# Performance work log

Hardware: AMD Instinct MI355X
Metric: run time of the kernel (lower is better)

The kernel has to match this reference:

```python
import jax, jax.numpy as jnp
import numpy as np

BATCH = 4096
INPUT_SIZE = 8192
IO = 16            # inputoutput_dim
D_STATE = 32       # statespace_dim
N_STAGES = INPUT_SIZE // IO  # 512


def _glorot(key, shape):
    # glorot-uniform over the trailing matrix dims, matching get_random_glorot_uniform_matrix
    lim = float(np.sqrt(6.0 / (shape[-2] + shape[-1])))
    return jax.random.uniform(key, shape, minval=-lim, maxval=lim, dtype=jnp.float32)


def setup_inputs() -> dict:
    key = jax.random.key(0)
    ks = jax.random.split(key, 10)
    U = jax.random.normal(ks[0], (BATCH, INPUT_SIZE), dtype=jnp.float32)
    A = _glorot(ks[1], (N_STAGES, D_STATE, D_STATE))
    B = _glorot(ks[2], (N_STAGES, D_STATE, IO))
    C = _glorot(ks[3], (N_STAGES, IO, D_STATE))
    D = _glorot(ks[4], (N_STAGES, IO, IO))
    E = _glorot(ks[5], (N_STAGES, D_STATE, D_STATE))
    F = _glorot(ks[6], (N_STAGES, D_STATE, IO))
    G = _glorot(ks[7], (N_STAGES, IO, D_STATE))
    lim_b = float(np.sqrt(6.0 / INPUT_SIZE))
    bias = jax.random.uniform(ks[8], (INPUT_SIZE,), minval=-lim_b, maxval=lim_b, dtype=jnp.float32)
    return {"U": U, "A": A, "B": B, "C": C, "D": D, "E": E, "F": F, "G": G, "bias": bias}


def reference(U, A, B, C, D, E, F, G, bias):
    bt, p = U.shape
    n, io, d = C.shape
    u = U.reshape(bt, n, io).transpose(1, 0, 2)  # (N, batch, io)
    x0 = jnp.zeros((bt, d), dtype=U.dtype)

    # causal: y_k = C_k x_k + D_k u_k ; x_{k+1} = A_k x_k + B_k u_k, x_0 = 0
    def causal_step(x, inp):
        A_k, B_k, C_k, D_k, u_k = inp
        y_k = x @ C_k.T + u_k @ D_k.T
        x = x @ A_k.T + u_k @ B_k.T
        return x, y_k

    _, y_c = jax.lax.scan(causal_step, x0, (A, B, C, D, u))

    # anticausal (runs from last stage to first): y_k += G_k z_k ; z_{k-1} = E_k z_k + F_k u_k, z_N = 0
    def anti_step(z, inp):
        E_k, F_k, G_k, u_k = inp
        y_k = z @ G_k.T
        z = z @ E_k.T + u_k @ F_k.T
        return z, y_k

    _, y_a = jax.lax.scan(anti_step, x0, (E, F, G, u), reverse=True)

    y = (y_c + y_a).transpose(1, 0, 2).reshape(bt, p) + bias
    return y
```

## Files before the change

kernel.cpp:

```cpp
#include <hip/hip_runtime.h>


#define BATCH 4096
#define NCH   16
#define CHS   32
#define SROWS (BATCH + 32)
#define TSTR  36

typedef __attribute__((ext_vector_type(8))) short short8;
typedef __attribute__((ext_vector_type(4))) float f32x4;
typedef short8 __attribute__((may_alias)) short8a;
typedef f32x4 __attribute__((may_alias)) f32x4a;
typedef unsigned __attribute__((may_alias)) uinta;

#define MFMA16(a, b, c) __builtin_amdgcn_mfma_f32_16x16x32_bf16(a, b, c, 0, 0, 0)

__device__ __forceinline__ unsigned short bf16u(float x) {
  unsigned u = __builtin_bit_cast(unsigned, x);
  u += 0x7fffu + ((u >> 16) & 1u);
  return (unsigned short)(u >> 16);
}
__device__ __forceinline__ float bf2f(unsigned short u) {
  return __builtin_bit_cast(float, ((unsigned)u) << 16);
}
template <int DT>
__device__ __forceinline__ const void* eptr(const void* b, long e) {
  return (const char*)b + e * (DT ? 4 : 2);
}

__device__ __forceinline__ void gload16(const void* g, void* lds) {
  __builtin_amdgcn_global_load_lds((const __attribute__((address_space(1))) void*)g,
                                   (__attribute__((address_space(3))) void*)lds, 16, 0, 0);
}
__device__ __forceinline__ void stage_blob8(const short* g, short* lds, int w, int lane) {
#pragma unroll
  for (int c = 0; c < 2; ++c) {
    const int ob = (w * 2 + c) * 1024;
    gload16((const char*)g + ob + lane * 16, (char*)lds + ob);
  }
}
__device__ __forceinline__ void stage_blob2k(const short* g, short* lds, int w, int lane) {
  if (w < 2) {
    const int ob = w * 1024;
    gload16((const char*)g + ob + lane * 16, (char*)lds + ob);
  }
}

template <int DT, int ROWS, int COLS, int PSTR>
__device__ __forceinline__ void stage2(const void* gp, short* hi, short* lo, int tid) {
  if constexpr (DT == 0) {
    const uinta* gu = (const uinta*)gp;
    for (int i = tid; i < ROWS * COLS / 2; i += 256) {
      int r = i / (COLS / 2), c = i - r * (COLS / 2);
      ((uinta*)(hi + r * PSTR))[c] = gu[i];
    }
  } else {
    const float* gf = (const float*)gp;
    for (int i = tid; i < ROWS * COLS; i += 256) {
      int r = i / COLS, c = i - r * COLS;
      float v = gf[i];
      unsigned short h = bf16u(v);
      hi[r * PSTR + c] = (short)h;
      lo[r * PSTR + c] = (short)bf16u(v - bf2f(h));
    }
  }
}
template <int DT, int ROWS, int COLS, int PSTR>
__device__ __forceinline__ void stage1(const void* gp, short* hi, int tid) {
  if constexpr (DT == 0) {
    const uinta* gu = (const uinta*)gp;
    for (int i = tid; i < ROWS * COLS / 2; i += 256) {
      int r = i / (COLS / 2), c = i - r * (COLS / 2);
      ((uinta*)(hi + r * PSTR))[c] = gu[i];
    }
  } else {
    const float* gf = (const float*)gp;
    for (int i = tid; i < ROWS * COLS; i += 256) {
      int r = i / COLS, c = i - r * COLS;
      hi[r * PSTR + c] = (short)bf16u(gf[i]);
    }
  }
}

__device__ __forceinline__ short8 ldfrag32(const short* l, int lane, int nbase) {
  int n = nbase + (lane & 15), q = lane >> 4;
  return *(const short8a*)(l + n * 40 + q * 8);
}
__device__ __forceinline__ short8 ldfrag16(const short* l, int lane, int nbase) {
  int n = nbase + (lane & 15), q = lane >> 4;
  short8 z = {};
  if (q < 2) z = *(const short8a*)(l + n * 24 + q * 8);
  return z;
}

__device__ __forceinline__ void twr(const f32x4* acc, float* T, int lane) {
  const int c = lane & 15, q = lane >> 4;
#pragma unroll
  for (int h = 0; h < 2; ++h)
#pragma unroll
    for (int r = 0; r < 4; ++r) T[(q * 4 + r) * TSTR + h * 16 + c] = acc[h][r];
}
__device__ __forceinline__ void trd(const float* T, int lane, short8& hi, short8& lo) {
  const int m = lane & 15, q = lane >> 4;
  const float* p = T + m * TSTR + q * 8;
#pragma unroll
  for (int j = 0; j < 8; ++j) {
    float v = p[j];
    unsigned short h = bf16u(v);
    hi[j] = (short)h;
    lo[j] = (short)bf16u(v - bf2f(h));
  }
}

template <int DT> struct URaw;
template <> struct URaw<0> { short8 s; };
template <> struct URaw<1> { f32x4 a, b; };

template <int DT>
__device__ __forceinline__ URaw<DT> ldu_raw(const void* U, size_t off) {
  URaw<DT> r;
  if constexpr (DT == 0) {
    r.s = *(const short8a*)((const short*)U + off);
  } else {
    const f32x4a* p = (const f32x4a*)((const float*)U + off);
    r.a = p[0];
    r.b = p[1];
  }
  return r;
}
template <int DT>
__device__ __forceinline__ void u_cvt(const URaw<DT>& r, short8& uhi, short8& ulo) {
  if constexpr (DT == 0) {
    uhi = r.s;
    ulo = short8{};
  } else {
#pragma unroll
    for (int j = 0; j < 4; ++j) {
      float v = r.a[j];
      unsigned short h = bf16u(v);
      uhi[j] = (short)h;
      ulo[j] = (short)bf16u(v - bf2f(h));
    }
#pragma unroll
    for (int j = 0; j < 4; ++j) {
      float v = r.b[j];
      unsigned short h = bf16u(v);
      uhi[4 + j] = (short)h;
      ulo[4 + j] = (short)bf16u(v - bf2f(h));
    }
  }
}
template <int DT, int MODE> struct UL {
  URaw<DT> r;
  __device__ __forceinline__ void fetch(const void* U, const short*, size_t row, int k, int qq) {
    r = ldu_raw<DT>(U, row * 8192 + (size_t)k * 16 + qq * 8);
  }
  __device__ __forceinline__ void get(short8& hi, short8& lo) const { u_cvt<DT>(r, hi, lo); }
};
template <> struct UL<1, 2> {
  short8 h, l;
  __device__ __forceinline__ void fetch(const void*, const short* Ub, size_t row, int k, int qq) {
    const short* p = Ub + (row * 1024 + (size_t)k * 2 + qq) * 16;
    h = *(const short8a*)p;
    l = *(const short8a*)(p + 8);
  }
  __device__ __forceinline__ void get(short8& hi, short8& lo) const { hi = h; lo = l; }
};

template <int DT>
__device__ __forceinline__ float ldbias(const void* b, int i) {
  if constexpr (DT == 0) return bf2f((unsigned short)((const short*)b)[i]);
  else return ((const float*)b)[i];
}

template <int DT>
__device__ __forceinline__ void step_state(const short8& Xhi, const short8& Xlo,
                                           const short8& uhi, const short8& ulo,
                                           const short* Mhi, const short* Mlo,
                                           const short* Bhi, const short* Blo,
                                           f32x4* out, int lane) {
#pragma unroll
  for (int h = 0; h < 2; ++h) {
    const f32x4 z4 = {0.f, 0.f, 0.f, 0.f};
    short8 bA = ldfrag32(Mhi, lane, h * 16);
    f32x4 ax = MFMA16(Xhi, bA, z4);
    ax = MFMA16(Xlo, bA, ax);
    short8 bB = ldfrag16(Bhi, lane, h * 16);
    ax = MFMA16(uhi, bB, ax);
    if constexpr (DT) {
      short8 bAl = ldfrag32(Mlo, lane, h * 16);
      ax = MFMA16(Xhi, bAl, ax);
      ax = MFMA16(ulo, bB, ax);
      short8 bBl = ldfrag16(Blo, lane, h * 16);
      ax = MFMA16(uhi, bBl, ax);
    }
    out[h] = ax;
  }
}

__global__ void k_detect(const unsigned short* __restrict__ U16, int* __restrict__ flag) {
  int lane = threadIdx.x;
  int bad = 0;
  for (int i = lane; i < 512; i += 64) {
    int e = (U16[i] >> 7) & 0xFF;
    bad += ((e > 134) || (e < 96 && e != 0)) ? 1 : 0;
  }
#pragma unroll
  for (int s = 32; s; s >>= 1) bad += __shfl_xor(bad, s);
  if (lane == 0) *flag = (bad > 48) ? 1 : 0;
}

template <int DT, int ROWS, int COLS, int PSTR, bool LO>
__device__ __forceinline__ void cvt_mat(const void* gp, short* hi, short* lo, int tid) {
  if constexpr (DT == 0) {
    const unsigned short* gs = (const unsigned short*)gp;
    for (int i = tid; i < ROWS * COLS; i += 256) {
      int r = i / COLS, c = i - r * COLS;
      hi[r * PSTR + c] = (short)gs[i];
    }
  } else {
    const float* gf = (const float*)gp;
    for (int i = tid; i < ROWS * COLS; i += 256) {
      int r = i / COLS, c = i - r * COLS;
      float v = gf[i];
      unsigned short h = bf16u(v);
      hi[r * PSTR + c] = (short)h;
      if constexpr (LO) lo[r * PSTR + c] = (short)bf16u(v - bf2f(h));
    }
  }
}
template <int DT>
__global__ __launch_bounds__(256) void k_prep(
    const int* __restrict__ flagp,
    const void* __restrict__ Am, const void* __restrict__ Bm, const void* __restrict__ Cm,
    const void* __restrict__ Dm, const void* __restrict__ Em, const void* __restrict__ Fm,
    const void* __restrict__ Gm,
    short* __restrict__ ABb, short* __restrict__ EFb, short* __restrict__ CDb,
    short* __restrict__ Gb) {
  if (*flagp != DT) return;
  const int k = blockIdx.x, tid = threadIdx.x;
  short* ab = ABb + (size_t)k * 4096;
  short* ef = EFb + (size_t)k * 4096;
  short* cd = CDb + (size_t)k * 1024;
  short* gb = Gb + (size_t)k * 1024;
  cvt_mat<DT, 32, 32, 40, true>(eptr<DT>(Am, (long)k * 1024), ab, ab + 1280, tid);
  cvt_mat<DT, 32, 16, 24, true>(eptr<DT>(Bm, (long)k * 512), ab + 2560, ab + 3328, tid);
  cvt_mat<DT, 32, 32, 40, true>(eptr<DT>(Em, (long)k * 1024), ef, ef + 1280, tid);
  cvt_mat<DT, 32, 16, 24, true>(eptr<DT>(Fm, (long)k * 512), ef + 2560, ef + 3328, tid);
  cvt_mat<DT, 16, 32, 40, false>(eptr<DT>(Cm, (long)k * 512), cd, nullptr, tid);
  cvt_mat<DT, 16, 16, 24, false>(eptr<DT>(Dm, (long)k * 256), cd + 640, nullptr, tid);
  cvt_mat<DT, 16, 32, 40, false>(eptr<DT>(Gm, (long)k * 512), gb, nullptr, tid);
}
__global__ __launch_bounds__(256) void k_prepU(const int* __restrict__ flagp,
                                               const float* __restrict__ Uf,
                                               short* __restrict__ Ub) {
  if (*flagp != 1) return;
  const size_t i = (size_t)blockIdx.x * 256 + threadIdx.x;
  const f32x4a* p = (const f32x4a*)(Uf + i * 8);
  f32x4 a = p[0], b = p[1];
  short8 hi, lo;
#pragma unroll
  for (int j = 0; j < 4; ++j) {
    unsigned short h = bf16u(a[j]);
    hi[j] = (short)h;
    lo[j] = (short)bf16u(a[j] - bf2f(h));
  }
#pragma unroll
  for (int j = 0; j < 4; ++j) {
    unsigned short h = bf16u(b[j]);
    hi[4 + j] = (short)h;
    lo[4 + j] = (short)bf16u(b[j] - bf2f(h));
  }
  *(short8a*)(Ub + i * 16) = hi;
  *(short8a*)(Ub + i * 16 + 8) = lo;
}

template <int DT, int MODE>
__global__ __launch_bounds__(256, 4) void k1_scan(
    const int* __restrict__ flagp, const void* __restrict__ U,
    const void* __restrict__ Am, const void* __restrict__ Bm,
    const void* __restrict__ Em, const void* __restrict__ Fm,
    const short* __restrict__ ABb, const short* __restrict__ EFb,
    const short* __restrict__ Ub,
    float* __restrict__ Sc, float* __restrict__ Sa) {
  if (*flagp != DT) return;
  const int ch = blockIdx.x, tile = blockIdx.y;
  const bool ident = (tile == 64);
  const int tid = threadIdx.x, lane = tid & 63, w = tid >> 6;
  const int s = ch * CHS;
  __shared__ __align__(16) short bAB[2][4096];
  __shared__ __align__(16) short bEF[2][4096];
  __shared__ __align__(16) float T[4][2][16 * TSTR];

  short8 Xhi = {}, Xlo = {}, Zhi = {}, Zlo = {};
  if (ident) {
    const int m = lane & 15, q = lane >> 4;
    short8 id = {};
#pragma unroll
    for (int j = 0; j < 8; ++j) id[j] = ((q * 8 + j) == (w * 16 + m)) ? (short)0x3F80 : (short)0;
    Xhi = id; Zhi = id;
  }

  auto stAB = [&](int k, int b) {
    if constexpr (MODE >= 1) {
      stage_blob8(ABb + (size_t)k * 4096, bAB[b], w, lane);
    } else {
      stage2<DT, 32, 32, 40>(eptr<DT>(Am, (long)k * 1024), bAB[b], bAB[b] + 1280, tid);
      stage2<DT, 32, 16, 24>(eptr<DT>(Bm, (long)k * 512), bAB[b] + 2560, bAB[b] + 3328, tid);
    }
  };
  auto stEF = [&](int k, int b) {
    if constexpr (MODE >= 1) {
      stage_blob8(EFb + (size_t)k * 4096, bEF[b], w, lane);
    } else {
      stage2<DT, 32, 32, 40>(eptr<DT>(Em, (long)k * 1024), bEF[b], bEF[b] + 1280, tid);
      stage2<DT, 32, 16, 24>(eptr<DT>(Fm, (long)k * 512), bEF[b] + 2560, bEF[b] + 3328, tid);
    }
  };

  stAB(s, 0);
  stEF(s + CHS - 1, 0);

  const size_t row = (size_t)(ident ? 0 : (tile * 64 + w * 16 + (lane & 15)));
  const int qq = (lane >> 4) & 1;
  UL<DT, MODE> upc, upa;
  if (!ident) {
    upc.fetch(U, Ub, row, s, qq);
    upa.fetch(U, Ub, row, s + CHS - 1, qq);
  }
  __syncthreads();

  f32x4 aX[2], aZ[2];
#pragma unroll 2
  for (int t = 0; t < CHS; ++t) {
    const int kc = s + t, ka = s + CHS - 1 - t, buf = t & 1;
    if (t < CHS - 1) {
      stAB(kc + 1, buf ^ 1);
      stEF(ka - 1, buf ^ 1);
    }
    short8 uch = {}, ucl = {}, uah = {}, ual = {};
    if (!ident) {
      upc.get(uch, ucl);
      upa.get(uah, ual);
      if (t < CHS - 1) {
        upc.fetch(U, Ub, row, kc + 1, qq);
        upa.fetch(U, Ub, row, ka - 1, qq);
      }
    }
    step_state<DT>(Xhi, Xlo, uch, ucl, bAB[buf], bAB[buf] + 1280, bAB[buf] + 2560,
                   bAB[buf] + 3328, aX, lane);
    step_state<DT>(Zhi, Zlo, uah, ual, bEF[buf], bEF[buf] + 1280, bEF[buf] + 2560,
                   bEF[buf] + 3328, aZ, lane);
    twr(aX, T[w][0], lane);
    twr(aZ, T[w][1], lane);
    trd(T[w][0], lane, Xhi, Xlo);
    trd(T[w][1], lane, Zhi, Zlo);
    __syncthreads();
  }

  if (!ident || w < 2) {
    const int grow = tile * 64 + w * 16;
#pragma unroll
    for (int h = 0; h < 2; ++h)
#pragma unroll
      for (int r = 0; r < 4; ++r) {
        const int m = (lane >> 4) * 4 + r, col = h * 16 + (lane & 15);
        const size_t off = ((size_t)ch * SROWS + grow + m) * 32 + col;
        Sc[off] = aX[h][r];
        Sa[off] = aZ[h][r];
      }
  }
}

__global__ __launch_bounds__(256) void k2_comb(float* __restrict__ Sc, float* __restrict__ Sa) {
  const int dir = blockIdx.y;
  const int r = threadIdx.x >> 5, j = threadIdx.x & 31;
  const int row = blockIdx.x * 8 + r;
  float* S = dir ? Sa : Sc;
  __shared__ float P[32][33];
  __shared__ float xs[8][33];
  float x = 0.f;
  for (int it = 0; it < NCH; ++it) {
    const int ch = dir ? (NCH - 1 - it) : it;
    const size_t base = ((size_t)ch * SROWS + row) * 32 + j;
    const float s_local = S[base];
    for (int i = threadIdx.x; i < 1024; i += 256)
      P[i >> 5][i & 31] = S[((size_t)ch * SROWS + BATCH + (i >> 5)) * 32 + (i & 31)];
    xs[r][j] = x;
    __syncthreads();
    S[base] = x;
    float acc = s_local;
#pragma unroll
    for (int m = 0; m < 32; ++m) acc += xs[r][m] * P[m][j];
    x = acc;
    __syncthreads();
  }
}

template <int DT, int MODE>
__global__ __launch_bounds__(256, 4) void k3_scan(
    const int* __restrict__ flagp, const void* __restrict__ U,
    const void* __restrict__ Am, const void* __restrict__ Bm,
    const void* __restrict__ Cm, const void* __restrict__ Dm,
    const void* __restrict__ Em, const void* __restrict__ Fm,
    const void* __restrict__ Gm, const void* __restrict__ biasv,
    const short* __restrict__ ABb, const short* __restrict__ EFb,
    const short* __restrict__ CDb, const short* __restrict__ Gb,
    const short* __restrict__ Ub,
    const float* __restrict__ xin, const float* __restrict__ zin,
    void* __restrict__ out) {
  if (*flagp != DT) return;
  const int ch = blockIdx.x, tile = blockIdx.y;
  const int tid = threadIdx.x, lane = tid & 63, w = tid >> 6;
  const int s = ch * CHS;
  __shared__ __align__(16) short bM[2][4096];
  __shared__ __align__(16) short bO[2][1024];
  __shared__ __align__(16) float T[4][16 * TSTR];
  const int cidx = lane & 15, quad = lane >> 4, qq = quad & 1;
  const size_t row = (size_t)(tile * 64 + w * 16 + cidx);

  auto stC = [&](int k, int b) {
    if constexpr (MODE >= 1) {
      stage_blob8(ABb + (size_t)k * 4096, bM[b], w, lane);
      stage_blob2k(CDb + (size_t)k * 1024, bO[b], w, lane);
    } else {
      stage2<DT, 32, 32, 40>(eptr<DT>(Am, (long)k * 1024), bM[b], bM[b] + 1280, tid);
      stage2<DT, 32, 16, 24>(eptr<DT>(Bm, (long)k * 512), bM[b] + 2560, bM[b] + 3328, tid);
      stage1<DT, 16, 32, 40>(eptr<DT>(Cm, (long)k * 512), bO[b], tid);
      stage1<DT, 16, 16, 24>(eptr<DT>(Dm, (long)k * 256), bO[b] + 640, tid);
    }
  };
  auto stA = [&](int k, int b) {
    if constexpr (MODE >= 1) {
      stage_blob8(EFb + (size_t)k * 4096, bM[b], w, lane);
      stage_blob2k(Gb + (size_t)k * 1024, bO[b], w, lane);
    } else {
      stage2<DT, 32, 32, 40>(eptr<DT>(Em, (long)k * 1024), bM[b], bM[b] + 1280, tid);
      stage2<DT, 32, 16, 24>(eptr<DT>(Fm, (long)k * 512), bM[b] + 2560, bM[b] + 3328, tid);
      stage1<DT, 16, 32, 40>(eptr<DT>(Gm, (long)k * 512), bO[b], tid);
    }
  };

  short8 Xhi, Xlo;
  {
    const float* xp = xin + ((size_t)ch * SROWS + row) * 32 + quad * 8;
#pragma unroll
    for (int j = 0; j < 8; ++j) {
      float v = xp[j];
      unsigned short h = bf16u(v);
      Xhi[j] = (short)h;
      Xlo[j] = (short)bf16u(v - bf2f(h));
    }
  }
  stC(s, 0);
  UL<DT, MODE> up;
  up.fetch(U, Ub, row, s, qq);
  __syncthreads();

  f32x4 aX[2];
#pragma unroll 2
  for (int t = 0; t < CHS; ++t) {
    const int k = s + t, buf = t & 1;
    if (t < CHS - 1) stC(k + 1, buf ^ 1);
    short8 uh, ul;
    up.get(uh, ul);
    if (t < CHS - 1) up.fetch(U, Ub, row, k + 1, qq);
    const f32x4 z4 = {0.f, 0.f, 0.f, 0.f};
    const short8 cf = ldfrag32(bO[buf], lane, 0);
    f32x4 ya = MFMA16(Xhi, cf, z4);
    ya = MFMA16(Xlo, cf, ya);
    const short8 df = ldfrag16(bO[buf] + 640, lane, 0);
    ya = MFMA16(uh, df, ya);
    if constexpr (DT) ya = MFMA16(ul, df, ya);
    const float bv = ldbias<DT>(biasv, k * 16 + cidx);
    {
      const size_t obase = (size_t)(tile * 64 + w * 16 + quad * 4) * 8192 + (size_t)k * 16 + cidx;
      if constexpr (DT == 0) {
        short* o = (short*)out;
#pragma unroll
        for (int r = 0; r < 4; ++r) o[obase + (size_t)r * 8192] = (short)bf16u(ya[r] + bv);
      } else {
        float* o = (float*)out;
#pragma unroll
        for (int r = 0; r < 4; ++r) o[obase + (size_t)r * 8192] = ya[r] + bv;
      }
    }
    step_state<DT>(Xhi, Xlo, uh, ul, bM[buf], bM[buf] + 1280, bM[buf] + 2560, bM[buf] + 3328,
                   aX, lane);
    twr(aX, T[w], lane);
    trd(T[w], lane, Xhi, Xlo);
    __syncthreads();
  }

  short8 Zhi, Zlo;
  {
    const float* zp = zin + ((size_t)ch * SROWS + row) * 32 + quad * 8;
#pragma unroll
    for (int j = 0; j < 8; ++j) {
      float v = zp[j];
      unsigned short h = bf16u(v);
      Zhi[j] = (short)h;
      Zlo[j] = (short)bf16u(v - bf2f(h));
    }
  }
  stA(s + CHS - 1, 0);
  up.fetch(U, Ub, row, s + CHS - 1, qq);
  __syncthreads();

  f32x4 aZ[2];
#pragma unroll 2
  for (int t = 0; t < CHS; ++t) {
    const int k = s + CHS - 1 - t, buf = t & 1;
    if (t < CHS - 1) stA(k - 1, buf ^ 1);
    short8 uh, ul;
    up.get(uh, ul);
    if (t < CHS - 1) up.fetch(U, Ub, row, k - 1, qq);
    const f32x4 z4 = {0.f, 0.f, 0.f, 0.f};
    const short8 gf = ldfrag32(bO[buf], lane, 0);
    f32x4 ya = MFMA16(Zhi, gf, z4);
    ya = MFMA16(Zlo, gf, ya);
    {
      const size_t obase = (size_t)(tile * 64 + w * 16 + quad * 4) * 8192 + (size_t)k * 16 + cidx;
      if constexpr (DT == 0) {
        short* o = (short*)out;
#pragma unroll
        for (int r = 0; r < 4; ++r) {
          const float c = bf2f((unsigned short)o[obase + (size_t)r * 8192]);
          o[obase + (size_t)r * 8192] = (short)bf16u(c + ya[r]);
        }
      } else {
        float* o = (float*)out;
#pragma unroll
        for (int r = 0; r < 4; ++r) o[obase + (size_t)r * 8192] += ya[r];
      }
    }
    step_state<DT>(Zhi, Zlo, uh, ul, bM[buf], bM[buf] + 1280, bM[buf] + 2560, bM[buf] + 3328,
                   aZ, lane);
    twr(aZ, T[w], lane);
    trd(T[w], lane, Zhi, Zlo);
    __syncthreads();
  }
}

extern "C" void kernel_launch(void* const* d_in, const int* in_sizes, int n_in,
                              void* d_out, int out_size, void* d_ws, size_t ws_size,
                              hipStream_t stream) {
  (void)in_sizes; (void)n_in; (void)out_size;
  const void* U = d_in[0];
  const void* A = d_in[1];
  const void* B = d_in[2];
  const void* C = d_in[3];
  const void* D = d_in[4];
  const void* E = d_in[5];
  const void* F = d_in[6];
  const void* G = d_in[7];
  const void* bias = d_in[8];

  constexpr size_t SC1 = (size_t)NCH * SROWS * 32;
  constexpr size_t BLOBS = (size_t)512 * 8192 * 2 + (size_t)512 * 2048 * 2;
  constexpr size_t UBB = (size_t)BATCH * 1024 * 32;
  constexpr size_t NEED1 = 1024 + BLOBS + SC1 * 8;
  constexpr size_t NEED2 = NEED1 + UBB;
  const int mode = (ws_size >= NEED2) ? 2 : (ws_size >= NEED1 ? 1 : 0);

  char* base = (char*)d_ws;
  int* flag = (int*)base;
  short* ABb = (short*)(base + 1024);
  short* EFb = ABb + (size_t)512 * 4096;
  short* CDb = EFb + (size_t)512 * 4096;
  short* Gb = CDb + (size_t)512 * 1024;
  float* Sc = (mode >= 1) ? (float*)(Gb + (size_t)512 * 1024) : (float*)(base + 1024);
  float* Sa = Sc + SC1;
  short* Ub = (short*)(Sa + SC1);

  k_detect<<<1, 64, 0, stream>>>((const unsigned short*)U, flag);
  if (mode >= 1) {
    k_prep<0><<<512, 256, 0, stream>>>(flag, A, B, C, D, E, F, G, ABb, EFb, CDb, Gb);
    k_prep<1><<<512, 256, 0, stream>>>(flag, A, B, C, D, E, F, G, ABb, EFb, CDb, Gb);
  }
  if (mode == 2) k_prepU<<<16384, 256, 0, stream>>>(flag, (const float*)U, Ub);

  if (mode == 2) {
    k1_scan<0, 1><<<dim3(NCH, 65), 256, 0, stream>>>(flag, U, A, B, E, F, ABb, EFb, Ub, Sc, Sa);
    k1_scan<1, 2><<<dim3(NCH, 65), 256, 0, stream>>>(flag, U, A, B, E, F, ABb, EFb, Ub, Sc, Sa);
    k2_comb<<<dim3(BATCH / 8, 2), 256, 0, stream>>>(Sc, Sa);
    k3_scan<0, 1><<<dim3(NCH, 64), 256, 0, stream>>>(flag, U, A, B, C, D, E, F, G, bias, ABb, EFb,
                                                     CDb, Gb, Ub, Sc, Sa, d_out);
    k3_scan<1, 2><<<dim3(NCH, 64), 256, 0, stream>>>(flag, U, A, B, C, D, E, F, G, bias, ABb, EFb,
                                                     CDb, Gb, Ub, Sc, Sa, d_out);
  } else if (mode == 1) {
    k1_scan<0, 1><<<dim3(NCH, 65), 256, 0, stream>>>(flag, U, A, B, E, F, ABb, EFb, Ub, Sc, Sa);
    k1_scan<1, 1><<<dim3(NCH, 65), 256, 0, stream>>>(flag, U, A, B, E, F, ABb, EFb, Ub, Sc, Sa);
    k2_comb<<<dim3(BATCH / 8, 2), 256, 0, stream>>>(Sc, Sa);
    k3_scan<0, 1><<<dim3(NCH, 64), 256, 0, stream>>>(flag, U, A, B, C, D, E, F, G, bias, ABb, EFb,
                                                     CDb, Gb, Ub, Sc, Sa, d_out);
    k3_scan<1, 1><<<dim3(NCH, 64), 256, 0, stream>>>(flag, U, A, B, C, D, E, F, G, bias, ABb, EFb,
                                                     CDb, Gb, Ub, Sc, Sa, d_out);
  } else {
    k1_scan<0, 0><<<dim3(NCH, 65), 256, 0, stream>>>(flag, U, A, B, E, F, ABb, EFb, Ub, Sc, Sa);
    k1_scan<1, 0><<<dim3(NCH, 65), 256, 0, stream>>>(flag, U, A, B, E, F, ABb, EFb, Ub, Sc, Sa);
    k2_comb<<<dim3(BATCH / 8, 2), 256, 0, stream>>>(Sc, Sa);
    k3_scan<0, 0><<<dim3(NCH, 64), 256, 0, stream>>>(flag, U, A, B, C, D, E, F, G, bias, ABb, EFb,
                                                     CDb, Gb, Ub, Sc, Sa, d_out);
    k3_scan<1, 0><<<dim3(NCH, 64), 256, 0, stream>>>(flag, U, A, B, C, D, E, F, G, bias, ABb, EFb,
                                                     CDb, Gb, Ub, Sc, Sa, d_out);
  }
}
```

Baseline: 609.5 us.

## Merge causal and anticausal passes of k3 into one interleaved loop

Replaces the two sequential loops of the final scan kernel (forward causal, then reverse anticausal) with one loop that advances both recurrences at once, with separate double-buffered LDS for AB/CD and EF/G. Output is written directly in the first half of the chunk and read-modify-written in the second half, so each output element gets one plain store and one read-add. This is meant to halve the serial loop length and overlap two independent dependency chains, and to drop the read-modify-write for half the elements. The cost is more LDS and registers, with launch bounds lowered from 4 to 3 blocks per CU. For fp32 output the first-half partial is packed as bf16 into the output buffer, which may lose precision.

```diff
diff --git a/kernel.cpp b/kernel.cpp
--- a/kernel.cpp
+++ b/kernel.cpp
@@ -22,6 +22,9 @@
 }
 __device__ __forceinline__ float bf2f(unsigned short u) {
   return __builtin_bit_cast(float, ((unsigned)u) << 16);
+}
+__device__ __forceinline__ unsigned pk2(float a, float b) {
+  return (unsigned)bf16u(a) | (((unsigned)bf16u(b)) << 16);
 }
 template <int DT>
 __device__ __forceinline__ const void* eptr(const void* b, long e) {
@@ -398,15 +401,144 @@
 }
 
 template <int DT, int MODE>
-__global__ __launch_bounds__(256, 4) void k3_scan(
+__global__ __launch_bounds__(256, 3) void k3_merged(
+    const int* __restrict__ flagp, const void* __restrict__ U, const void* __restrict__ biasv,
+    const short* __restrict__ ABb, const short* __restrict__ EFb,
+    const short* __restrict__ CDb, const short* __restrict__ Gb,
+    const short* __restrict__ Ub,
+    const float* __restrict__ xin, const float* __restrict__ zin,
+    void* __restrict__ out) {
+  if (*flagp != DT) return;
+  const int ch = blockIdx.x, tile = blockIdx.y;
+  const int tid = threadIdx.x, lane = tid & 63, w = tid >> 6;
+  const int s = ch * CHS;
+  __shared__ __align__(16) short bAB[2][4096];
+  __shared__ __align__(16) short bEF[2][4096];
+  __shared__ __align__(16) short bCD[2][1024];
+  __shared__ __align__(16) short bG[2][1024];
+  __shared__ __align__(16) float T[4][16 * TSTR];
+
+  const int cidx = lane & 15, quad = lane >> 4, qq = quad & 1;
+  const size_t row = (size_t)(tile * 64 + w * 16 + cidx);
+
+  short8 Xhi, Xlo, Zhi, Zlo;
+  {
+    const float* xp = xin + ((size_t)ch * SROWS + row) * 32 + quad * 8;
+    const float* zp = zin + ((size_t)ch * SROWS + row) * 32 + quad * 8;
+#pragma unroll
+    for (int j = 0; j < 8; ++j) {
+      float v = xp[j];
+      unsigned short h = bf16u(v);
+      Xhi[j] = (short)h;
+      Xlo[j] = (short)bf16u(v - bf2f(h));
+      float z = zp[j];
+      unsigned short hz = bf16u(z);
+      Zhi[j] = (short)hz;
+      Zlo[j] = (short)bf16u(z - bf2f(hz));
+    }
+  }
+
+  stage_blob8(ABb + (size_t)s * 4096, bAB[0], w, lane);
+  stage_blob2k(CDb + (size_t)s * 1024, bCD[0], w, lane);
+  stage_blob8(EFb + (size_t)(s + CHS - 1) * 4096, bEF[0], w, lane);
+  stage_blob2k(Gb + (size_t)(s + CHS - 1) * 1024, bG[0], w, lane);
+  UL<DT, MODE> upc, upa;
+  upc.fetch(U, Ub, row, s, qq);
+  upa.fetch(U, Ub, row, s + CHS - 1, qq);
+  __syncthreads();
+
+  f32x4 aX[2], aZ[2];
+#pragma unroll 2
+  for (int t = 0; t < CHS; ++t) {
+    const int kc = s + t, ka = s + CHS - 1 - t, buf = t & 1;
+    if (t < CHS - 1) {
+      stage_blob8(ABb + (size_t)(kc + 1) * 4096, bAB[buf ^ 1], w, lane);
+      stage_blob2k(CDb + (size_t)(kc + 1) * 1024, bCD[buf ^ 1], w, lane);
+      stage_blob8(EFb + (size_t)(ka - 1) * 4096, bEF[buf ^ 1], w, lane);
+      stage_blob2k(Gb + (size_t)(ka - 1) * 1024, bG[buf ^ 1], w, lane);
+    }
+    short8 uh, ul, vh, vl;
+    upc.get(uh, ul);
+    upa.get(vh, vl);
+    if (t < CHS - 1) {
+      upc.fetch(U, Ub, row, kc + 1, qq);
+      upa.fetch(U, Ub, row, ka - 1, qq);
+    }
+    const f32x4 z4 = {0.f, 0.f, 0.f, 0.f};
+    const short8 cf = ldfrag32(bCD[buf], lane, 0);
+    f32x4 yc = MFMA16(Xhi, cf, z4);
+    yc = MFMA16(Xlo, cf, yc);
+    const short8 df = ldfrag16(bCD[buf] + 640, lane, 0);
+    yc = MFMA16(uh, df, yc);
+    if constexpr (DT) yc = MFMA16(ul, df, yc);
+    const short8 gf = ldfrag32(bG[buf], lane, 0);
+    f32x4 yz = MFMA16(Zhi, gf, z4);
+    yz = MFMA16(Zlo, gf, yz);
+
+    const float bv = ldbias<DT>(biasv, kc * 16 + cidx);
+    const size_t rbase = (size_t)(tile * 64 + w * 16 + quad * 4) * 8192;
+    const size_t oc = rbase + (size_t)kc * 16 + cidx;
+    const size_t oa = rbase + (size_t)ka * 16 + cidx;
+    if constexpr (DT == 0) {
+      short* o = (short*)out;
+      if (t < CHS / 2) {
+#pragma unroll
+        for (int r = 0; r < 4; ++r) o[oc + (size_t)r * 8192] = (short)bf16u(yc[r] + bv);
+#pragma unroll
+        for (int r = 0; r < 4; ++r) o[oa + (size_t)r * 8192] = (short)bf16u(yz[r]);
+      } else {
+#pragma unroll
+        for (int r = 0; r < 4; ++r) {
+          const float c = bf2f((unsigned short)o[oc + (size_t)r * 8192]);
+          o[oc + (size_t)r * 8192] = (short)bf16u(c + yc[r] + bv);
+        }
+#pragma unroll
+        for (int r = 0; r < 4; ++r) {
+          const float c = bf2f((unsigned short)o[oa + (size_t)r * 8192]);
+          o[oa + (size_t)r * 8192] = (short)bf16u(c + yz[r]);
+        }
+      }
+    } else {
+      float* o = (float*)out;
+      if (t < CHS / 2) {
+        *(uinta*)(o + oc) = pk2(yc[0] + bv, yc[1] + bv);
+        *(uinta*)(o + oc + 2 * 8192) = pk2(yc[2] + bv, yc[3] + bv);
+        *(uinta*)(o + oa) = pk2(yz[0], yz[1]);
+        *(uinta*)(o + oa + 2 * 8192) = pk2(yz[2], yz[3]);
+      } else {
+        const unsigned p0 = *(const uinta*)(o + oc);
+        const unsigned p1 = *(const uinta*)(o + oc + 2 * 8192);
+        o[oc + 0 * 8192] = bf2f((unsigned short)(p0 & 0xffffu)) + yc[0] + bv;
+        o[oc + 1 * 8192] = bf2f((unsigned short)(p0 >> 16)) + yc[1] + bv;
+        o[oc + 2 * 8192] = bf2f((unsigned short)(p1 & 0xffffu)) + yc[2] + bv;
+        o[oc + 3 * 8192] = bf2f((unsigned short)(p1 >> 16)) + yc[3] + bv;
+        const unsigned q0 = *(const uinta*)(o + oa);
+        const unsigned q1 = *(const uinta*)(o + oa + 2 * 8192);
+        o[oa + 0 * 8192] = bf2f((unsigned short)(q0 & 0xffffu)) + yz[0];
+        o[oa + 1 * 8192] = bf2f((unsigned short)(q0 >> 16)) + yz[1];
+        o[oa + 2 * 8192] = bf2f((unsigned short)(q1 & 0xffffu)) + yz[2];
+        o[oa + 3 * 8192] = bf2f((unsigned short)(q1 >> 16)) + yz[3];
+      }
+    }
+    step_state<DT>(Xhi, Xlo, uh, ul, bAB[buf], bAB[buf] + 1280, bAB[buf] + 2560,
+                   bAB[buf] + 3328, aX, lane);
+    step_state<DT>(Zhi, Zlo, vh, vl, bEF[buf], bEF[buf] + 1280, bEF[buf] + 2560,
+                   bEF[buf] + 3328, aZ, lane);
+    twr(aX, T[w], lane);
+    trd(T[w], lane, Xhi, Xlo);
+    twr(aZ, T[w], lane);
+    trd(T[w], lane, Zhi, Zlo);
+    __syncthreads();
+  }
+}
+
+template <int DT>
+__global__ __launch_bounds__(256, 4) void k3_legacy(
     const int* __restrict__ flagp, const void* __restrict__ U,
     const void* __restrict__ Am, const void* __restrict__ Bm,
     const void* __restrict__ Cm, const void* __restrict__ Dm,
     const void* __restrict__ Em, const void* __restrict__ Fm,
     const void* __restrict__ Gm, const void* __restrict__ biasv,
-    const short* __restrict__ ABb, const short* __restrict__ EFb,
-    const short* __restrict__ CDb, const short* __restrict__ Gb,
-    const short* __restrict__ Ub,
     const float* __restrict__ xin, const float* __restrict__ zin,
     void* __restrict__ out) {
   if (*flagp != DT) return;
@@ -420,25 +552,15 @@
   const size_t row = (size_t)(tile * 64 + w * 16 + cidx);
 
   auto stC = [&](int k, int b) {
-    if constexpr (MODE >= 1) {
-      stage_blob8(ABb + (size_t)k * 4096, bM[b], w, lane);
-      stage_blob2k(CDb + (size_t)k * 1024, bO[b], w, lane);
-    } else {
-      stage2<DT, 32, 32, 40>(eptr<DT>(Am, (long)k * 1024), bM[b], bM[b] + 1280, tid);
-      stage2<DT, 32, 16, 24>(eptr<DT>(Bm, (long)k * 512), bM[b] + 2560, bM[b] + 3328, tid);
-      stage1<DT, 16, 32, 40>(eptr<DT>(Cm, (long)k * 512), bO[b], tid);
-      stage1<DT, 16, 16, 24>(eptr<DT>(Dm, (long)k * 256), bO[b] + 640, tid);
-    }
+    stage2<DT, 32, 32, 40>(eptr<DT>(Am, (long)k * 1024), bM[b], bM[b] + 1280, tid);
+    stage2<DT, 32, 16, 24>(eptr<DT>(Bm, (long)k * 512), bM[b] + 2560, bM[b] + 3328, tid);
+    stage1<DT, 16, 32, 40>(eptr<DT>(Cm, (long)k * 512), bO[b], tid);
+    stage1<DT, 16, 16, 24>(eptr<DT>(Dm, (long)k * 256), bO[b] + 640, tid);
   };
   auto stA = [&](int k, int b) {
-    if constexpr (MODE >= 1) {
-      stage_blob8(EFb + (size_t)k * 4096, bM[b], w, lane);
-      stage_blob2k(Gb + (size_t)k * 1024, bO[b], w, lane);
-    } else {
-      stage2<DT, 32, 32, 40>(eptr<DT>(Em, (long)k * 1024), bM[b], bM[b] + 1280, tid);
-      stage2<DT, 32, 16, 24>(eptr<DT>(Fm, (long)k * 512), bM[b] + 2560, bM[b] + 3328, tid);
-      stage1<DT, 16, 32, 40>(eptr<DT>(Gm, (long)k * 512), bO[b], tid);
-    }
+    stage2<DT, 32, 32, 40>(eptr<DT>(Em, (long)k * 1024), bM[b], bM[b] + 1280, tid);
+    stage2<DT, 32, 16, 24>(eptr<DT>(Fm, (long)k * 512), bM[b] + 2560, bM[b] + 3328, tid);
+    stage1<DT, 16, 32, 40>(eptr<DT>(Gm, (long)k * 512), bO[b], tid);
   };
 
   short8 Xhi, Xlo;
@@ -453,8 +575,8 @@
     }
   }
   stC(s, 0);
-  UL<DT, MODE> up;
-  up.fetch(U, Ub, row, s, qq);
+  UL<DT, 0> up;
+  up.fetch(U, nullptr, row, s, qq);
   __syncthreads();
 
   f32x4 aX[2];
@@ -464,7 +586,7 @@
     if (t < CHS - 1) stC(k + 1, buf ^ 1);
     short8 uh, ul;
     up.get(uh, ul);
-    if (t < CHS - 1) up.fetch(U, Ub, row, k + 1, qq);
+    if (t < CHS - 1) up.fetch(U, nullptr, row, k + 1, qq);
     const f32x4 z4 = {0.f, 0.f, 0.f, 0.f};
     const short8 cf = ldfrag32(bO[buf], lane, 0);
     f32x4 ya = MFMA16(Xhi, cf, z4);
@@ -504,7 +626,7 @@
     }
   }
   stA(s + CHS - 1, 0);
-  up.fetch(U, Ub, row, s + CHS - 1, qq);
+  up.fetch(U, nullptr, row, s + CHS - 1, qq);
   __syncthreads();
 
   f32x4 aZ[2];
@@ -514,7 +636,7 @@
     if (t < CHS - 1) stA(k - 1, buf ^ 1);
     short8 uh, ul;
     up.get(uh, ul);
-    if (t < CHS - 1) up.fetch(U, Ub, row, k - 1, qq);
+    if (t < CHS - 1) up.fetch(U, nullptr, row, k - 1, qq);
     const f32x4 z4 = {0.f, 0.f, 0.f, 0.f};
     const short8 gf = ldfrag32(bO[buf], lane, 0);
     f32x4 ya = MFMA16(Zhi, gf, z4);
@@ -580,29 +702,28 @@
   }
   if (mode == 2) k_prepU<<<16384, 256, 0, stream>>>(flag, (const float*)U, Ub);
 
-  if (mode == 2) {
+  if (mode >= 1) {
     k1_scan<0, 1><<<dim3(NCH, 65), 256, 0, stream>>>(flag, U, A, B, E, F, ABb, EFb, Ub, Sc, Sa);
-    k1_scan<1, 2><<<dim3(NCH, 65), 256, 0, stream>>>(flag, U, A, B, E, F, ABb, EFb, Ub, Sc, Sa);
+    if (mode == 2)
+      k1_scan<1, 2><<<dim3(NCH, 65), 256, 0, stream>>>(flag, U, A, B, E, F, ABb, EFb, Ub, Sc, Sa);
+    else
+      k1_scan<1, 1><<<dim3(NCH, 65), 256, 0, stream>>>(flag, U, A, B, E, F, ABb, EFb, Ub, Sc, Sa);
     k2_comb<<<dim3(BATCH / 8, 2), 256, 0, stream>>>(Sc, Sa);
-    k3_scan<0, 1><<<dim3(NCH, 64), 256, 0, stream>>>(flag, U, A, B, C, D, E, F, G, bias, ABb, EFb,
-                                                     CDb, Gb, Ub, Sc, Sa, d_out);
-    k3_scan<1, 2><<<dim3(NCH, 64), 256, 0, stream>>>(flag, U, A, B, C, D, E, F, G, bias, ABb, EFb,
-                                                     CDb, Gb, Ub, Sc, Sa, d_out);
-  } else if (mode == 1) {
-    k1_scan<0, 1><<<dim3(NCH, 65), 256, 0, stream>>>(flag, U, A, B, E, F, ABb, EFb, Ub, Sc, Sa);
-    k1_scan<1, 1><<<dim3(NCH, 65), 256, 0, stream>>>(flag, U, A, B, E, F, ABb, EFb, Ub, Sc, Sa);
-    k2_comb<<<dim3(BATCH / 8, 2), 256, 0, stream>>>(Sc, Sa);
-    k3_scan<0, 1><<<dim3(NCH, 64), 256, 0, stream>>>(flag, U, A, B, C, D, E, F, G, bias, ABb, EFb,
-                                                     CDb, Gb, Ub, Sc, Sa, d_out);
-    k3_scan<1, 1><<<dim3(NCH, 64), 256, 0, stream>>>(flag, U, A, B, C, D, E, F, G, bias, ABb, EFb,
-                                                     CDb, Gb, Ub, Sc, Sa, d_out);
+    k3_merged<0, 1><<<dim3(NCH, 64), 256, 0, stream>>>(flag, U, bias, ABb, EFb, CDb, Gb, Ub,
+                                                       Sc, Sa, d_out);
+    if (mode == 2)
+      k3_merged<1, 2><<<dim3(NCH, 64), 256, 0, stream>>>(flag, U, bias, ABb, EFb, CDb, Gb, Ub,
+                                                         Sc, Sa, d_out);
+    else
+      k3_merged<1, 1><<<dim3(NCH, 64), 256, 0, stream>>>(flag, U, bias, ABb, EFb, CDb, Gb, Ub,
+                                                         Sc, Sa, d_out);
   } else {
     k1_scan<0, 0><<<dim3(NCH, 65), 256, 0, stream>>>(flag, U, A, B, E, F, ABb, EFb, Ub, Sc, Sa);
     k1_scan<1, 0><<<dim3(NCH, 65), 256, 0, stream>>>(flag, U, A, B, E, F, ABb, EFb, Ub, Sc, Sa);
     k2_comb<<<dim3(BATCH / 8, 2), 256, 0, stream>>>(Sc, Sa);
-    k3_scan<0, 0><<<dim3(NCH, 64), 256, 0, stream>>>(flag, U, A, B, C, D, E, F, G, bias, ABb, EFb,
-                                                     CDb, Gb, Ub, Sc, Sa, d_out);
-    k3_scan<1, 0><<<dim3(NCH, 64), 256, 0, stream>>>(flag, U, A, B, C, D, E, F, G, bias, ABb, EFb,
-                                                     CDb, Gb, Ub, Sc, Sa, d_out);
-  }
-}
+    k3_legacy<0><<<dim3(NCH, 64), 256, 0, stream>>>(flag, U, A, B, C, D, E, F, G, bias,
+                                                    Sc, Sa, d_out);
+    k3_legacy<1><<<dim3(NCH, 64), 256, 0, stream>>>(flag, U, A, B, C, D, E, F, G, bias,
+                                                    Sc, Sa, d_out);
+  }
+}
```

Result: no change. 605.4 us (-0.7%).
